# Performance work log

Hardware: AMD Instinct MI355X
Metric: run time of the kernel (lower is better)

The kernel has to match this reference:

```python
import jax, jax.numpy as jnp
import numpy as np

N_NODES, N_GRAPHS, HIDDEN, N_BRANCH = 131072, 4096, 512, 4
G_HEAD, N_HEAD = 50, 3  # graph head dim, node head dim; var_output=1 doubles MLP output


def setup_inputs() -> dict:
    key = jax.random.key(0)
    ks = jax.random.split(key, 10)
    s = 0.02
    x = jax.random.normal(ks[0], (N_NODES, HIDDEN), dtype=jnp.float32)
    # sorted graph assignment: 32 nodes per graph (consecutive, as unique_consecutive assumes)
    batch = (jnp.arange(N_NODES) // (N_NODES // N_GRAPHS)).astype(jnp.int32)
    dataset_ids = jax.random.randint(ks[1], (N_GRAPHS,), 0, N_BRANCH).astype(jnp.int32)
    return {
        "x": x,
        "Ws": jax.random.normal(ks[2], (N_BRANCH, HIDDEN, HIDDEN)) * s,
        "bs": jnp.zeros((N_BRANCH, HIDDEN)),
        "Wg": jax.random.normal(ks[3], (N_BRANCH, HIDDEN, 2 * G_HEAD)) * s,
        "bg": jnp.zeros((N_BRANCH, 2 * G_HEAD)),
        "Wn1": jax.random.normal(ks[4], (N_BRANCH, HIDDEN, HIDDEN)) * s,
        "bn1": jnp.zeros((N_BRANCH, HIDDEN)),
        "Wn2": jax.random.normal(ks[5], (N_BRANCH, HIDDEN, 2 * N_HEAD)) * s,
        "bn2": jnp.zeros((N_BRANCH, 2 * N_HEAD)),
        "batch": batch,
        "dataset_ids": dataset_ids,
    }


def reference(x, Ws, bs, Wg, bg, Wn1, bn1, Wn2, bn2, batch, dataset_ids):
    n_graphs = dataset_ids.shape[0]
    n_branch = Ws.shape[0]
    ghd = Wg.shape[2] // 2
    nhd = Wn2.shape[2] // 2
    # mean pooling per graph (graph_pool_fn with 'mean' reduction)
    ones = jnp.ones((x.shape[0],), dtype=x.dtype)
    counts = jax.ops.segment_sum(ones, batch, num_segments=n_graphs)
    x_graph = jax.ops.segment_sum(x, batch, num_segments=n_graphs) / counts[:, None]
    node_ds = dataset_ids[batch]  # per-node branch id (repeat_interleave of graph mask)

    g_head = jnp.zeros((n_graphs, ghd), dtype=x.dtype)
    g_var = jnp.zeros((n_graphs, ghd), dtype=x.dtype)
    n_head_out = jnp.zeros((x.shape[0], nhd), dtype=x.dtype)
    n_var = jnp.zeros((x.shape[0], nhd), dtype=x.dtype)
    for b in range(n_branch):  # fixed small branch set (structurally distinct experts)
        # graph head branch: graph_shared MLP -> head MLP, scatter back via mask
        hg = jax.nn.relu(x_graph @ Ws[b] + bs[b])
        og = hg @ Wg[b] + bg[b]
        mg = (dataset_ids == b).astype(x.dtype)[:, None]
        g_head = g_head + mg * og[:, :ghd]
        g_var = g_var + mg * (og[:, ghd:] ** 2)
        # node head branch (node_NN_type == 'mlp')
        hn = jax.nn.relu(x @ Wn1[b] + bn1[b])
        on = hn @ Wn2[b] + bn2[b]
        mn = (node_ds == b).astype(x.dtype)[:, None]
        n_head_out = n_head_out + mn * on[:, :nhd]
        n_var = n_var + mn * (on[:, nhd:] ** 2)
    return (g_head, g_var, n_head_out, n_var)
```

## Files before the change

kernel.cpp:

```cpp
#include <hip/hip_runtime.h>

#define N_NODES  131072
#define N_GRAPHS 4096
#define HID      512

typedef float  f32x4  __attribute__((ext_vector_type(4)));
typedef __bf16 bf16x8 __attribute__((ext_vector_type(8)));
typedef unsigned short u16x8 __attribute__((ext_vector_type(8)));

__device__ __forceinline__ unsigned short f2bf(float f) {
  unsigned int u = __builtin_bit_cast(unsigned int, f);
  u += 0x7FFFu + ((u >> 16) & 1u);
  return (unsigned short)(u >> 16);
}
__device__ __forceinline__ unsigned int pack2bf(float a, float b) {
  return (unsigned int)f2bf(a) | ((unsigned int)f2bf(b) << 16);
}
__device__ __forceinline__ f32x4 mfma_bf16(bf16x8 a, bf16x8 b, f32x4 c) {
  return __builtin_amdgcn_mfma_f32_16x16x32_bf16(a, b, c, 0, 0, 0);
}

__global__ __launch_bounds__(256) void bucket_kernel(
    const int* __restrict__ dsid, int* __restrict__ perm, int* __restrict__ meta) {
  __shared__ int cnt[4], base[4], off[4];
  int t = threadIdx.x;
  if (t < 4) { cnt[t] = 0; off[t] = 0; }
  __syncthreads();
  for (int g = t; g < N_GRAPHS; g += 256) atomicAdd(&cnt[dsid[g]], 1);
  __syncthreads();
  if (t == 0) {
    int s = 0;
    for (int b = 0; b < 4; ++b) { base[b] = s; s += cnt[b]; meta[b] = cnt[b]; }
  }
  __syncthreads();
  for (int g = t; g < N_GRAPHS; g += 256) {
    int b = dsid[g];
    int p = base[b] + atomicAdd(&off[b], 1);
    perm[p] = g;
  }
}

__global__ __launch_bounds__(256) void prep_wf_kernel(
    const float* __restrict__ Wn1, const float* __restrict__ Ws,
    unsigned short* __restrict__ W1Tf, unsigned short* __restrict__ WsTf) {
  __shared__ unsigned short lt[8192];
  const int bid = blockIdx.x;
  const int which = bid >> 7;
  const int b  = (bid >> 5) & 3;
  const int hf = bid & 31;
  const float* src = (which ? Ws : Wn1) + (size_t)b * 512 * 512 + hf * 16;
  unsigned short* dst = (which ? WsTf : W1Tf) + (size_t)(b * 32 + hf) * 8192;
  const int t = threadIdx.x;
  for (int i = t; i < 8192; i += 256) {
    int k = i >> 4;
    int n = i & 15;
    float v = src[(size_t)k * 512 + n];
    int kk = k >> 5, lane = n + ((k >> 3) & 3) * 16, e = k & 7;
    lt[(kk * 64 + lane) * 8 + e] = f2bf(v);
  }
  __syncthreads();
  u16x8* d8 = (u16x8*)dst;
  const u16x8* s8 = (const u16x8*)lt;
  for (int i = t; i < 1024; i += 256) d8[i] = s8[i];
}

__global__ __launch_bounds__(256) void prep_wg_kernel(
    const float* __restrict__ Wg, unsigned short* __restrict__ WgT) {
  int idx = blockIdx.x * 256 + threadIdx.x;
  int b = idx >> 16;
  int r = (idx >> 9) & 127;
  int k = idx & 511;
  float v = (r < 100) ? Wg[(b * 512 + k) * 100 + r] : 0.f;
  WgT[idx] = f2bf(v);
}

#define NT_MAX 2050
__global__ __launch_bounds__(512, 4) void node_kernel(
    const float* __restrict__ x,
    const int* __restrict__ meta,
    const int* __restrict__ perm,
    const unsigned short* __restrict__ W1Tf,
    const float* __restrict__ bn1,
    const float* __restrict__ Wn2,
    const float* __restrict__ bn2,
    unsigned short* __restrict__ xg,
    float* __restrict__ n_head,
    float* __restrict__ n_var) {
  __shared__ __align__(16) unsigned short xtile[4 * 16 * 512];
  __shared__ __align__(16) float red[8][64][6];

  const int4 cv = *(const int4*)meta;
  const int cnts[4] = {cv.x, cv.y, cv.z, cv.w};

  int i = blockIdx.x, branch = -1, permOff = 0, nvalid = 0, pb = 0;
  for (int b = 0; b < 4; ++b) {
    int nt = (cnts[b] + 1) >> 1;
    if (branch < 0 && i < nt) { branch = b; permOff = pb + i * 2; nvalid = min(2, cnts[b] - i * 2); }
    if (branch < 0) i -= nt;
    pb += cnts[b];
  }
  if (branch < 0) return;

  const int t    = threadIdx.x;
  const int lane = t & 63;
  const int w    = t >> 6;
  const int l15  = lane & 15;
  const int l4   = lane >> 4;

  const int g0 = perm[permOff];
  const int g1 = perm[permOff + (nvalid > 1 ? 1 : 0)];

  {
    const int gg = t >> 8;
    const int ci = (t & 255) * 2;
    const int g  = gg ? g1 : g0;
    const float* src = x + (size_t)g * 32 * HID + ci;
    const int kk = ci >> 5;
    const int ln = (ci >> 3) & 3;
    const int e  = ci & 7;
    float s0 = 0.f, s1 = 0.f;
    #pragma unroll 8
    for (int row = 0; row < 32; ++row) {
      float2 v = *(const float2*)(src + (size_t)row * HID);
      s0 += v.x; s1 += v.y;
      int rt = gg * 32 + row;
      int pos = (((rt >> 4) * 16 + kk) * 64 + ((rt & 15) + ln * 16)) * 8 + e;
      *(unsigned int*)&xtile[pos] = pack2bf(v.x, v.y);
    }
    if (gg == 0 || nvalid > 1)
      *(unsigned int*)&xg[(size_t)g * HID + ci] = pack2bf(s0 * (1.f / 32.f), s1 * (1.f / 32.f));
  }
  __syncthreads();

  f32x4 acc[4][4];
  #pragma unroll
  for (int m = 0; m < 4; ++m)
    #pragma unroll
    for (int n = 0; n < 4; ++n) acc[m][n] = (f32x4)0.f;

  const unsigned short* wbase = W1Tf + ((size_t)(branch * 32 + w * 4)) * 8192 + lane * 8;
  const unsigned short* xbase = xtile + lane * 8;

  #pragma unroll
  for (int kk = 0; kk < 16; ++kk) {
    bf16x8 af[4];
    #pragma unroll
    for (int m = 0; m < 4; ++m)
      af[m] = *(const bf16x8*)(wbase + (m * 16 + kk) * 512);
    bf16x8 bfr[4];
    #pragma unroll
    for (int n = 0; n < 4; ++n)
      bfr[n] = *(const bf16x8*)(xbase + (n * 16 + kk) * 512);
    #pragma unroll
    for (int m = 0; m < 4; ++m)
      #pragma unroll
      for (int n = 0; n < 4; ++n)
        acc[m][n] = mfma_bf16(af[m], bfr[n], acc[m][n]);
  }

  float part[4][6];
  #pragma unroll
  for (int n = 0; n < 4; ++n)
    #pragma unroll
    for (int j = 0; j < 6; ++j) part[n][j] = 0.f;
  const float* W2 = Wn2 + branch * HID * 6;
  const float* B1 = bn1 + branch * HID;
  #pragma unroll
  for (int m = 0; m < 4; ++m) {
    #pragma unroll
    for (int r = 0; r < 4; ++r) {
      int hcol = w * 64 + m * 16 + l4 * 4 + r;
      float b1 = B1[hcol];
      float w2[6];
      #pragma unroll
      for (int j = 0; j < 6; ++j) w2[j] = W2[hcol * 6 + j];
      #pragma unroll
      for (int n = 0; n < 4; ++n) {
        float h = fmaxf(acc[m][n][r] + b1, 0.f);
        #pragma unroll
        for (int j = 0; j < 6; ++j) part[n][j] += h * w2[j];
      }
    }
  }
  #pragma unroll
  for (int n = 0; n < 4; ++n)
    #pragma unroll
    for (int j = 0; j < 6; ++j) {
      part[n][j] += __shfl_xor(part[n][j], 16);
      part[n][j] += __shfl_xor(part[n][j], 32);
    }
  if (lane < 16) {
    #pragma unroll
    for (int n = 0; n < 4; ++n)
      #pragma unroll
      for (int j = 0; j < 6; ++j) red[w][n * 16 + l15][j] = part[n][j];
  }
  __syncthreads();
  if (t < 64) {
    int row = t;
    if (row < nvalid * 32) {
      int node = (row < 32 ? g0 : g1) * 32 + (row & 31);
      #pragma unroll
      for (int j = 0; j < 6; ++j) {
        float s = red[0][row][j] + red[1][row][j] + red[2][row][j] + red[3][row][j]
                + red[4][row][j] + red[5][row][j] + red[6][row][j] + red[7][row][j]
                + bn2[branch * 6 + j];
        if (j < 3) n_head[(size_t)node * 3 + j] = s;
        else       n_var[(size_t)node * 3 + (j - 3)] = s * s;
      }
    }
  }
}

#define GT_MAX 67
__global__ __launch_bounds__(512, 4) void gstage1_kernel(
    const unsigned short* __restrict__ xg,
    const int* __restrict__ meta,
    const int* __restrict__ perm,
    const unsigned short* __restrict__ WsTf,
    const float* __restrict__ bs_,
    unsigned short* __restrict__ hg) {
  __shared__ __align__(16) unsigned short xtile[4 * 16 * 512];
  __shared__ int gidl[64];

  const int4 cv = *(const int4*)meta;
  const int cnts[4] = {cv.x, cv.y, cv.z, cv.w};

  int i = blockIdx.x, branch = -1, permOff = 0, nvalid = 0, pb = 0;
  for (int b = 0; b < 4; ++b) {
    int gt = (cnts[b] + 63) >> 6;
    if (branch < 0 && i < gt) { branch = b; permOff = pb + i * 64; nvalid = min(64, cnts[b] - i * 64); }
    if (branch < 0) i -= gt;
    pb += cnts[b];
  }
  if (branch < 0) return;

  const int t    = threadIdx.x;
  const int lane = t & 63;
  const int w    = t >> 6;
  const int l15  = lane & 15;
  const int l4   = lane >> 4;

  if (t < 64) gidl[t] = perm[permOff + min(t, nvalid - 1)];
  __syncthreads();

  for (int idx = t; idx < 4096; idx += 512) {
    int row = idx >> 6;
    int c8  = (idx & 63) * 8;
    u16x8 v = *(const u16x8*)&xg[(size_t)gidl[row] * HID + c8];
    int kk = c8 >> 5, ln = (c8 >> 3) & 3;
    *(u16x8*)&xtile[(((row >> 4) * 16 + kk) * 64 + ((row & 15) + ln * 16)) * 8] = v;
  }
  __syncthreads();

  f32x4 acc[4][4];
  #pragma unroll
  for (int m = 0; m < 4; ++m)
    #pragma unroll
    for (int n = 0; n < 4; ++n) acc[m][n] = (f32x4)0.f;

  const unsigned short* wbase = WsTf + ((size_t)(branch * 32 + w * 4)) * 8192 + lane * 8;
  const unsigned short* xbase = xtile + lane * 8;
  #pragma unroll
  for (int kk = 0; kk < 16; ++kk) {
    bf16x8 af[4];
    #pragma unroll
    for (int m = 0; m < 4; ++m)
      af[m] = *(const bf16x8*)(wbase + (m * 16 + kk) * 512);
    bf16x8 bfr[4];
    #pragma unroll
    for (int n = 0; n < 4; ++n)
      bfr[n] = *(const bf16x8*)(xbase + (n * 16 + kk) * 512);
    #pragma unroll
    for (int m = 0; m < 4; ++m)
      #pragma unroll
      for (int n = 0; n < 4; ++n)
        acc[m][n] = mfma_bf16(af[m], bfr[n], acc[m][n]);
  }

  const float* B1 = bs_ + branch * HID;
  #pragma unroll
  for (int m = 0; m < 4; ++m) {
    #pragma unroll
    for (int n = 0; n < 4; ++n) {
      int row = n * 16 + l15;
      if (row < nvalid) {
        int g = gidl[row];
        int hcb = w * 64 + m * 16 + l4 * 4;
        ushort4 hv;
        hv.x = f2bf(fmaxf(acc[m][n][0] + B1[hcb + 0], 0.f));
        hv.y = f2bf(fmaxf(acc[m][n][1] + B1[hcb + 1], 0.f));
        hv.z = f2bf(fmaxf(acc[m][n][2] + B1[hcb + 2], 0.f));
        hv.w = f2bf(fmaxf(acc[m][n][3] + B1[hcb + 3], 0.f));
        *(ushort4*)(hg + (size_t)g * HID + hcb) = hv;
      }
    }
  }
}

#define G2_MAX 259
__global__ __launch_bounds__(256) void gstage2_kernel(
    const int* __restrict__ meta,
    const int* __restrict__ perm,
    const unsigned short* __restrict__ hg,
    const unsigned short* __restrict__ WgT,
    const float* __restrict__ bg,
    float* __restrict__ g_head,
    float* __restrict__ g_var) {
  __shared__ int gidl[16];
  const int4 cv = *(const int4*)meta;
  const int cnts[4] = {cv.x, cv.y, cv.z, cv.w};

  int i = blockIdx.x, branch = -1, permOff = 0, nvalid = 0, pb = 0;
  for (int b = 0; b < 4; ++b) {
    int gt = (cnts[b] + 15) >> 4;
    if (branch < 0 && i < gt) { branch = b; permOff = pb + i * 16; nvalid = min(16, cnts[b] - i * 16); }
    if (branch < 0) i -= gt;
    pb += cnts[b];
  }
  if (branch < 0) return;

  const int t    = threadIdx.x;
  const int lane = t & 63;
  const int w    = t >> 6;
  const int l15  = lane & 15;
  const int l4   = lane >> 4;

  if (t < 16) gidl[t] = perm[permOff + min(t, nvalid - 1)];
  __syncthreads();

  f32x4 acc2[2];
  acc2[0] = (f32x4)0.f; acc2[1] = (f32x4)0.f;
  const unsigned short* arow = hg + (size_t)gidl[l15] * HID + l4 * 8;
  const unsigned short* brow = WgT + ((size_t)branch * 128 + w * 32 + l15) * 512 + l4 * 8;
  #pragma unroll
  for (int ks = 0; ks < 16; ++ks) {
    bf16x8 a  = *(const bf16x8*)(arow + ks * 32);
    bf16x8 b0 = *(const bf16x8*)(brow + ks * 32);
    bf16x8 b1 = *(const bf16x8*)(brow + 16 * 512 + ks * 32);
    acc2[0] = mfma_bf16(a, b0, acc2[0]);
    acc2[1] = mfma_bf16(a, b1, acc2[1]);
  }
  #pragma unroll
  for (int n2 = 0; n2 < 2; ++n2) {
    int j = w * 32 + n2 * 16 + l15;
    if (j < 100) {
      float bias = bg[branch * 100 + j];
      #pragma unroll
      for (int rr = 0; rr < 4; ++rr) {
        int r = l4 * 4 + rr;
        if (r < nvalid) {
          int g = gidl[r];
          float val = acc2[n2][rr] + bias;
          if (j < 50) g_head[(size_t)g * 50 + j] = val;
          else        g_var[(size_t)g * 50 + (j - 50)] = val * val;
        }
      }
    }
  }
}

extern "C" void kernel_launch(void* const* d_in, const int* in_sizes, int n_in,
                              void* d_out, int out_size, void* d_ws, size_t ws_size,
                              hipStream_t stream) {
  const float* x    = (const float*)d_in[0];
  const float* Ws   = (const float*)d_in[1];
  const float* bs   = (const float*)d_in[2];
  const float* Wg   = (const float*)d_in[3];
  const float* bg   = (const float*)d_in[4];
  const float* Wn1  = (const float*)d_in[5];
  const float* bn1  = (const float*)d_in[6];
  const float* Wn2  = (const float*)d_in[7];
  const float* bn2  = (const float*)d_in[8];
  const int* dsid   = (const int*)d_in[10];

  float* out    = (float*)d_out;
  float* g_head = out;
  float* g_var  = out + (size_t)N_GRAPHS * 50;
  float* n_head = out + (size_t)2 * N_GRAPHS * 50;
  float* n_var  = n_head + (size_t)N_NODES * 3;

  char* ws = (char*)d_ws;
  int* perm = (int*)(ws);
  int* meta = (int*)(ws + 16384);
  unsigned short* W1Tf = (unsigned short*)(ws + 16640);
  unsigned short* WsTf = (unsigned short*)(ws + 2113792);
  unsigned short* WgT  = (unsigned short*)(ws + 4210944);
  unsigned short* xg   = (unsigned short*)(ws + 4735232);
  unsigned short* hg   = (unsigned short*)(ws + 8929536);
  if (ws_size < 13123840) return;

  bucket_kernel<<<dim3(1), dim3(256), 0, stream>>>(dsid, perm, meta);
  prep_wf_kernel<<<dim3(256), dim3(256), 0, stream>>>(Wn1, Ws, W1Tf, WsTf);
  prep_wg_kernel<<<dim3(1024), dim3(256), 0, stream>>>(Wg, WgT);
  node_kernel<<<dim3(NT_MAX), dim3(512), 0, stream>>>(
      x, meta, perm, W1Tf, bn1, Wn2, bn2, xg, n_head, n_var);
  gstage1_kernel<<<dim3(GT_MAX), dim3(512), 0, stream>>>(
      xg, meta, perm, WsTf, bs, hg);
  gstage2_kernel<<<dim3(G2_MAX), dim3(256), 0, stream>>>(
      meta, perm, hg, WgT, bg, g_head, g_var);
}
```

Baseline: 196.9 us.

## Pipeline node-kernel x loading with MFMA over double-buffered K chunks

The node kernel used to load the two graphs' 64x512 x tile, convert it to bf16 and stage it in LDS in one pass, then run all 16 K-steps of MFMA. It now walks the K dimension in four 128-column chunks through a double-buffered LDS fragment. Each chunk prefetches the next chunk's global loads while the current chunk's MFMAs run, and raises wave priority during the MFMA section. The graph mean-pooling sums are built per chunk with shuffles and a small LDS partial-sum buffer, and the output-reduction scratch now reuses the x fragment buffer. Together these roughly halve LDS use so more blocks may fit per CU, at the cost of four extra block barriers and more complex indexing.

```diff
diff --git a/kernel.cpp b/kernel.cpp
--- a/kernel.cpp
+++ b/kernel.cpp
@@ -12,9 +12,6 @@
   unsigned int u = __builtin_bit_cast(unsigned int, f);
   u += 0x7FFFu + ((u >> 16) & 1u);
   return (unsigned short)(u >> 16);
-}
-__device__ __forceinline__ unsigned int pack2bf(float a, float b) {
-  return (unsigned int)f2bf(a) | ((unsigned int)f2bf(b) << 16);
 }
 __device__ __forceinline__ f32x4 mfma_bf16(bf16x8 a, bf16x8 b, f32x4 c) {
   return __builtin_amdgcn_mfma_f32_16x16x32_bf16(a, b, c, 0, 0, 0);
@@ -86,12 +83,11 @@
     unsigned short* __restrict__ xg,
     float* __restrict__ n_head,
     float* __restrict__ n_var) {
-  __shared__ __align__(16) unsigned short xtile[4 * 16 * 512];
-  __shared__ __align__(16) float red[8][64][6];
-
-  const int4 cv = *(const int4*)meta;
-  const int cnts[4] = {cv.x, cv.y, cv.z, cv.w};
-
+  __shared__ __align__(16) unsigned short xfrag[2][8192];
+  __shared__ __align__(16) float psum[2][8][128];
+
+  const int4 cvv = *(const int4*)meta;
+  const int cnts[4] = {cvv.x, cvv.y, cvv.z, cvv.w};
   int i = blockIdx.x, branch = -1, permOff = 0, nvalid = 0, pb = 0;
   for (int b = 0; b < 4; ++b) {
     int nt = (cnts[b] + 1) >> 1;
@@ -110,27 +106,17 @@
   const int g0 = perm[permOff];
   const int g1 = perm[permOff + (nvalid > 1 ? 1 : 0)];
 
-  {
-    const int gg = t >> 8;
-    const int ci = (t & 255) * 2;
-    const int g  = gg ? g1 : g0;
-    const float* src = x + (size_t)g * 32 * HID + ci;
-    const int kk = ci >> 5;
-    const int ln = (ci >> 3) & 3;
-    const int e  = ci & 7;
-    float s0 = 0.f, s1 = 0.f;
-    #pragma unroll 8
-    for (int row = 0; row < 32; ++row) {
-      float2 v = *(const float2*)(src + (size_t)row * HID);
-      s0 += v.x; s1 += v.y;
-      int rt = gg * 32 + row;
-      int pos = (((rt >> 4) * 16 + kk) * 64 + ((rt & 15) + ln * 16)) * 8 + e;
-      *(unsigned int*)&xtile[pos] = pack2bf(v.x, v.y);
-    }
-    if (gg == 0 || nvalid > 1)
-      *(unsigned int*)&xg[(size_t)g * HID + ci] = pack2bf(s0 * (1.f / 32.f), s1 * (1.f / 32.f));
-  }
-  __syncthreads();
+  const int sg = t >> 8;
+  const int qq = (t >> 4) & 15;
+  const int o  = t & 15;
+  const int gsrc = sg ? g1 : g0;
+  const float* srow0 = x + ((size_t)gsrc * 32 + qq) * HID + o * 8;
+  const float* srow1 = srow0 + 16 * HID;
+  const int kkl = o >> 2, wl4 = o & 3;
+  const int wpos0 = ((sg * 2 + 0) * 4 + kkl) * 512 + (wl4 * 16 + qq) * 8;
+  const int wpos1 = ((sg * 2 + 1) * 4 + kkl) * 512 + (wl4 * 16 + qq) * 8;
+
+  const unsigned short* wbase = W1Tf + ((size_t)(branch * 32 + w * 4)) * 8192 + lane * 8;
 
   f32x4 acc[4][4];
   #pragma unroll
@@ -138,24 +124,71 @@
     #pragma unroll
     for (int n = 0; n < 4; ++n) acc[m][n] = (f32x4)0.f;
 
-  const unsigned short* wbase = W1Tf + ((size_t)(branch * 32 + w * 4)) * 8192 + lane * 8;
-  const unsigned short* xbase = xtile + lane * 8;
-
-  #pragma unroll
-  for (int kk = 0; kk < 16; ++kk) {
-    bf16x8 af[4];
-    #pragma unroll
-    for (int m = 0; m < 4; ++m)
-      af[m] = *(const bf16x8*)(wbase + (m * 16 + kk) * 512);
-    bf16x8 bfr[4];
-    #pragma unroll
-    for (int n = 0; n < 4; ++n)
-      bfr[n] = *(const bf16x8*)(xbase + (n * 16 + kk) * 512);
-    #pragma unroll
-    for (int m = 0; m < 4; ++m)
+  float4 p0 = *(const float4*)(srow0);
+  float4 p1 = *(const float4*)(srow0 + 4);
+  float4 p2 = *(const float4*)(srow1);
+  float4 p3 = *(const float4*)(srow1 + 4);
+
+  #pragma unroll
+  for (int c = 0; c < 4; ++c) {
+    u16x8 ua, ub;
+    ua[0]=f2bf(p0.x); ua[1]=f2bf(p0.y); ua[2]=f2bf(p0.z); ua[3]=f2bf(p0.w);
+    ua[4]=f2bf(p1.x); ua[5]=f2bf(p1.y); ua[6]=f2bf(p1.z); ua[7]=f2bf(p1.w);
+    ub[0]=f2bf(p2.x); ub[1]=f2bf(p2.y); ub[2]=f2bf(p2.z); ub[3]=f2bf(p2.w);
+    ub[4]=f2bf(p3.x); ub[5]=f2bf(p3.y); ub[6]=f2bf(p3.z); ub[7]=f2bf(p3.w);
+    *(u16x8*)&xfrag[c & 1][wpos0] = ua;
+    *(u16x8*)&xfrag[c & 1][wpos1] = ub;
+
+    float s[8];
+    s[0]=p0.x+p2.x; s[1]=p0.y+p2.y; s[2]=p0.z+p2.z; s[3]=p0.w+p2.w;
+    s[4]=p1.x+p3.x; s[5]=p1.y+p3.y; s[6]=p1.z+p3.z; s[7]=p1.w+p3.w;
+    #pragma unroll
+    for (int j = 0; j < 8; ++j) {
+      s[j] += __shfl_xor(s[j], 16);
+      s[j] += __shfl_xor(s[j], 32);
+    }
+    if (lane < 16) {
+      float4 a4; a4.x=s[0]; a4.y=s[1]; a4.z=s[2]; a4.w=s[3];
+      float4 b4; b4.x=s[4]; b4.y=s[5]; b4.z=s[6]; b4.w=s[7];
+      *(float4*)&psum[c & 1][w][lane * 8]     = a4;
+      *(float4*)&psum[c & 1][w][lane * 8 + 4] = b4;
+    }
+
+    if (c < 3) {
+      p0 = *(const float4*)(srow0 + (c + 1) * 128);
+      p1 = *(const float4*)(srow0 + (c + 1) * 128 + 4);
+      p2 = *(const float4*)(srow1 + (c + 1) * 128);
+      p3 = *(const float4*)(srow1 + (c + 1) * 128 + 4);
+    }
+    __syncthreads();
+
+    if (t < 256) {
+      int gg = t >> 7, cc = t & 127;
+      if (gg == 0 || nvalid > 1) {
+        float sv = psum[c & 1][gg * 4 + 0][cc] + psum[c & 1][gg * 4 + 1][cc]
+                 + psum[c & 1][gg * 4 + 2][cc] + psum[c & 1][gg * 4 + 3][cc];
+        xg[(size_t)(gg ? g1 : g0) * HID + c * 128 + cc] = f2bf(sv * (1.f / 32.f));
+      }
+    }
+
+    __builtin_amdgcn_s_setprio(1);
+    #pragma unroll
+    for (int kk = 0; kk < 4; ++kk) {
+      bf16x8 af[4];
+      #pragma unroll
+      for (int m = 0; m < 4; ++m)
+        af[m] = *(const bf16x8*)(wbase + (size_t)(m * 16 + c * 4 + kk) * 512);
+      bf16x8 bfr[4];
       #pragma unroll
       for (int n = 0; n < 4; ++n)
-        acc[m][n] = mfma_bf16(af[m], bfr[n], acc[m][n]);
+        bfr[n] = *(const bf16x8*)&xfrag[c & 1][(n * 4 + kk) * 512 + lane * 8];
+      #pragma unroll
+      for (int m = 0; m < 4; ++m)
+        #pragma unroll
+        for (int n = 0; n < 4; ++n)
+          acc[m][n] = mfma_bf16(af[m], bfr[n], acc[m][n]);
+    }
+    __builtin_amdgcn_s_setprio(0);
   }
 
   float part[4][6];
@@ -189,6 +222,7 @@
       part[n][j] += __shfl_xor(part[n][j], 16);
       part[n][j] += __shfl_xor(part[n][j], 32);
     }
+  float (*red)[64][6] = (float (*)[64][6])&xfrag[0][0];
   if (lane < 16) {
     #pragma unroll
     for (int n = 0; n < 4; ++n)
@@ -202,11 +236,11 @@
       int node = (row < 32 ? g0 : g1) * 32 + (row & 31);
       #pragma unroll
       for (int j = 0; j < 6; ++j) {
-        float s = red[0][row][j] + red[1][row][j] + red[2][row][j] + red[3][row][j]
-                + red[4][row][j] + red[5][row][j] + red[6][row][j] + red[7][row][j]
-                + bn2[branch * 6 + j];
-        if (j < 3) n_head[(size_t)node * 3 + j] = s;
-        else       n_var[(size_t)node * 3 + (j - 3)] = s * s;
+        float sv = red[0][row][j] + red[1][row][j] + red[2][row][j] + red[3][row][j]
+                 + red[4][row][j] + red[5][row][j] + red[6][row][j] + red[7][row][j]
+                 + bn2[branch * 6 + j];
+        if (j < 3) n_head[(size_t)node * 3 + j] = sv;
+        else       n_var[(size_t)node * 3 + (j - 3)] = sv * sv;
       }
     }
   }
```

Result: slower. 290.2 us (+47.4%).

## Restructure node kernel loads, swizzle LDS tile, and stream weight fragments per slice

Applied to the files above, without the earlier changes.

The node kernel's x loading now has each wave read 8 rows with 16-byte float4 loads and write 16-byte bf16 packets into an XOR-swizzled LDS tile, so reads avoid bank conflicts. Graph-mean partial sums are reduced through shared memory instead of per-thread column loops. The MLP GEMM is split into four sequential hidden-column slices per wave, each with a 4-deep rolling prefetch of weight fragments. This cuts accumulator registers from 64 to 16 floats, which may help occupancy. The cost is an extra barrier and reduction pass for the pooled sums.

```diff
diff --git a/kernel.cpp b/kernel.cpp
--- a/kernel.cpp
+++ b/kernel.cpp
@@ -12,9 +12,6 @@
   unsigned int u = __builtin_bit_cast(unsigned int, f);
   u += 0x7FFFu + ((u >> 16) & 1u);
   return (unsigned short)(u >> 16);
-}
-__device__ __forceinline__ unsigned int pack2bf(float a, float b) {
-  return (unsigned int)f2bf(a) | ((unsigned int)f2bf(b) << 16);
 }
 __device__ __forceinline__ f32x4 mfma_bf16(bf16x8 a, bf16x8 b, f32x4 c) {
   return __builtin_amdgcn_mfma_f32_16x16x32_bf16(a, b, c, 0, 0, 0);
@@ -86,12 +83,11 @@
     unsigned short* __restrict__ xg,
     float* __restrict__ n_head,
     float* __restrict__ n_var) {
-  __shared__ __align__(16) unsigned short xtile[4 * 16 * 512];
-  __shared__ __align__(16) float red[8][64][6];
+  __shared__ __align__(16) unsigned short xtile[32768];
+  __shared__ __align__(16) float psum[8][8][64];
 
   const int4 cv = *(const int4*)meta;
   const int cnts[4] = {cv.x, cv.y, cv.z, cv.w};
-
   int i = blockIdx.x, branch = -1, permOff = 0, nvalid = 0, pb = 0;
   for (int b = 0; b < 4; ++b) {
     int nt = (cnts[b] + 1) >> 1;
@@ -102,86 +98,91 @@
   if (branch < 0) return;
 
   const int t    = threadIdx.x;
-  const int lane = t & 63;
+  const int l    = t & 63;
   const int w    = t >> 6;
-  const int l15  = lane & 15;
-  const int l4   = lane >> 4;
-
-  const int g0 = perm[permOff];
-  const int g1 = perm[permOff + (nvalid > 1 ? 1 : 0)];
-
-  {
-    const int gg = t >> 8;
-    const int ci = (t & 255) * 2;
-    const int g  = gg ? g1 : g0;
-    const float* src = x + (size_t)g * 32 * HID + ci;
-    const int kk = ci >> 5;
-    const int ln = (ci >> 3) & 3;
-    const int e  = ci & 7;
-    float s0 = 0.f, s1 = 0.f;
-    #pragma unroll 8
-    for (int row = 0; row < 32; ++row) {
-      float2 v = *(const float2*)(src + (size_t)row * HID);
-      s0 += v.x; s1 += v.y;
-      int rt = gg * 32 + row;
-      int pos = (((rt >> 4) * 16 + kk) * 64 + ((rt & 15) + ln * 16)) * 8 + e;
-      *(unsigned int*)&xtile[pos] = pack2bf(v.x, v.y);
-    }
-    if (gg == 0 || nvalid > 1)
-      *(unsigned int*)&xg[(size_t)g * HID + ci] = pack2bf(s0 * (1.f / 32.f), s1 * (1.f / 32.f));
-  }
-  __syncthreads();
-
-  f32x4 acc[4][4];
-  #pragma unroll
-  for (int m = 0; m < 4; ++m)
-    #pragma unroll
-    for (int n = 0; n < 4; ++n) acc[m][n] = (f32x4)0.f;
-
-  const unsigned short* wbase = W1Tf + ((size_t)(branch * 32 + w * 4)) * 8192 + lane * 8;
-  const unsigned short* xbase = xtile + lane * 8;
-
-  #pragma unroll
-  for (int kk = 0; kk < 16; ++kk) {
-    bf16x8 af[4];
-    #pragma unroll
-    for (int m = 0; m < 4; ++m)
-      af[m] = *(const bf16x8*)(wbase + (m * 16 + kk) * 512);
-    bf16x8 bfr[4];
-    #pragma unroll
-    for (int n = 0; n < 4; ++n)
-      bfr[n] = *(const bf16x8*)(xbase + (n * 16 + kk) * 512);
-    #pragma unroll
-    for (int m = 0; m < 4; ++m)
-      #pragma unroll
-      for (int n = 0; n < 4; ++n)
-        acc[m][n] = mfma_bf16(af[m], bfr[n], acc[m][n]);
-  }
+  const int l15  = l & 15;
+  const int l4   = l >> 4;
+  const int q    = w >> 2;
+  const int gidw = perm[permOff + min(q, nvalid - 1)];
+
+  float ps[8];
+  #pragma unroll
+  for (int e = 0; e < 8; ++e) ps[e] = 0.f;
+  const float* src = x + ((size_t)gidw * 32 + (w & 3) * 8) * HID + l * 8;
+  const int wkk = l >> 2, wl4 = l & 3;
+  #pragma unroll
+  for (int ii = 0; ii < 8; ++ii) {
+    float4 p0 = *(const float4*)(src + (size_t)ii * HID);
+    float4 p1 = *(const float4*)(src + (size_t)ii * HID + 4);
+    int row = w * 8 + ii, n = row >> 4, r15 = row & 15;
+    u16x8 ua;
+    ua[0]=f2bf(p0.x); ua[1]=f2bf(p0.y); ua[2]=f2bf(p0.z); ua[3]=f2bf(p0.w);
+    ua[4]=f2bf(p1.x); ua[5]=f2bf(p1.y); ua[6]=f2bf(p1.z); ua[7]=f2bf(p1.w);
+    *(u16x8*)&xtile[(((n * 16 + wkk) * 64) + (wl4 << 4) + (r15 ^ wkk)) * 8] = ua;
+    ps[0]+=p0.x; ps[1]+=p0.y; ps[2]+=p0.z; ps[3]+=p0.w;
+    ps[4]+=p1.x; ps[5]+=p1.y; ps[6]+=p1.z; ps[7]+=p1.w;
+  }
+  #pragma unroll
+  for (int e = 0; e < 8; ++e) psum[w][e][l] = ps[e];
+  __syncthreads();
+
+  #pragma unroll
+  for (int h = 0; h < 2; ++h) {
+    int c = t + h * 512;
+    int qq = c >> 9, cq = c & 511;
+    if (qq < nvalid) {
+      int oct = cq >> 3, e = cq & 7;
+      float sv = psum[qq * 4 + 0][e][oct] + psum[qq * 4 + 1][e][oct]
+               + psum[qq * 4 + 2][e][oct] + psum[qq * 4 + 3][e][oct];
+      xg[(size_t)perm[permOff + qq] * HID + cq] = f2bf(sv * (1.f / 32.f));
+    }
+  }
+  __syncthreads();
 
   float part[4][6];
   #pragma unroll
   for (int n = 0; n < 4; ++n)
     #pragma unroll
     for (int j = 0; j < 6; ++j) part[n][j] = 0.f;
+  const float* B1 = bn1 + branch * HID;
   const float* W2 = Wn2 + branch * HID * 6;
-  const float* B1 = bn1 + branch * HID;
-  #pragma unroll
-  for (int m = 0; m < 4; ++m) {
+
+  #pragma unroll
+  for (int s = 0; s < 4; ++s) {
+    const int hf = s * 8 + w;
+    const unsigned short* wb = W1Tf + ((size_t)(branch * 32 + hf)) * 8192 + l * 8;
+    f32x4 acc[4];
+    acc[0] = (f32x4)0.f; acc[1] = (f32x4)0.f; acc[2] = (f32x4)0.f; acc[3] = (f32x4)0.f;
+    bf16x8 afr[4];
+    #pragma unroll
+    for (int k2 = 0; k2 < 4; ++k2) afr[k2] = *(const bf16x8*)(wb + k2 * 512);
+    #pragma unroll
+    for (int kk = 0; kk < 16; ++kk) {
+      bf16x8 af = afr[kk & 3];
+      if (kk < 12) afr[kk & 3] = *(const bf16x8*)(wb + (kk + 4) * 512);
+      const int slot = (l4 << 4) | (l15 ^ kk);
+      #pragma unroll
+      for (int n = 0; n < 4; ++n) {
+        bf16x8 bfr = *(const bf16x8*)&xtile[(((n * 16 + kk) * 64) + slot) * 8];
+        acc[n] = mfma_bf16(af, bfr, acc[n]);
+      }
+    }
     #pragma unroll
     for (int r = 0; r < 4; ++r) {
-      int hcol = w * 64 + m * 16 + l4 * 4 + r;
+      int hcol = hf * 16 + l4 * 4 + r;
       float b1 = B1[hcol];
       float w2[6];
       #pragma unroll
       for (int j = 0; j < 6; ++j) w2[j] = W2[hcol * 6 + j];
       #pragma unroll
       for (int n = 0; n < 4; ++n) {
-        float h = fmaxf(acc[m][n][r] + b1, 0.f);
+        float h = fmaxf(acc[n][r] + b1, 0.f);
         #pragma unroll
         for (int j = 0; j < 6; ++j) part[n][j] += h * w2[j];
       }
     }
   }
+
   #pragma unroll
   for (int n = 0; n < 4; ++n)
     #pragma unroll
@@ -189,7 +190,8 @@
       part[n][j] += __shfl_xor(part[n][j], 16);
       part[n][j] += __shfl_xor(part[n][j], 32);
     }
-  if (lane < 16) {
+  float (*red)[64][6] = (float (*)[64][6])&psum[0][0][0];
+  if (l < 16) {
     #pragma unroll
     for (int n = 0; n < 4; ++n)
       #pragma unroll
@@ -197,16 +199,16 @@
   }
   __syncthreads();
   if (t < 64) {
-    int row = t;
-    if (row < nvalid * 32) {
-      int node = (row < 32 ? g0 : g1) * 32 + (row & 31);
+    int qq = t >> 5;
+    if (qq < nvalid) {
+      int node = perm[permOff + qq] * 32 + (t & 31);
       #pragma unroll
       for (int j = 0; j < 6; ++j) {
-        float s = red[0][row][j] + red[1][row][j] + red[2][row][j] + red[3][row][j]
-                + red[4][row][j] + red[5][row][j] + red[6][row][j] + red[7][row][j]
-                + bn2[branch * 6 + j];
-        if (j < 3) n_head[(size_t)node * 3 + j] = s;
-        else       n_var[(size_t)node * 3 + (j - 3)] = s * s;
+        float sv = bn2[branch * 6 + j];
+        #pragma unroll
+        for (int k = 0; k < 8; ++k) sv += red[k][t][j];
+        if (j < 3) n_head[(size_t)node * 3 + j] = sv;
+        else       n_var[(size_t)node * 3 + (j - 3)] = sv * sv;
       }
     }
   }
```

Result: slower. 232.2 us (+17.9%).
